# Kernel tuning notes

Hardware: AMD Instinct MI355X
Metric: run time of the kernel (lower is better)

## Reference

```python
import jax, jax.numpy as jnp
import numpy as np

D_MODEL = 1024
NUM_HEADS = 16
HEAD_DIM = D_MODEL // NUM_HEADS


def setup_inputs() -> dict:
    key = jax.random.key(0)
    ks = jax.random.split(key, 11)
    B, S, D = 2, 2048, D_MODEL
    s = 1.0 / np.sqrt(D)
    return {
        "query": jax.random.normal(ks[0], (B, S, D), jnp.float32),
        "key": jax.random.normal(ks[1], (B, S, D), jnp.float32),
        "value": jax.random.normal(ks[2], (B, S, D), jnp.float32),
        "w_q": jax.random.normal(ks[3], (D, D), jnp.float32) * s,
        "b_q": jnp.zeros((D,), jnp.float32),
        "w_k": jax.random.normal(ks[4], (D, D), jnp.float32) * s,
        "b_k": jnp.zeros((D,), jnp.float32),
        "w_v": jax.random.normal(ks[5], (D, D), jnp.float32) * s,
        "b_v": jnp.zeros((D,), jnp.float32),
        "w_o": jax.random.normal(ks[6], (D, D), jnp.float32) * s,
        "b_o": jnp.zeros((D,), jnp.float32),
    }


def reference(query, key, value, w_q, b_q, w_k, b_k, w_v, b_v, w_o, b_o):
    B, S, D = query.shape
    H, Hd = NUM_HEADS, HEAD_DIM
    # Linear layers (torch convention: x @ W.T + b)
    Q = (query @ w_q.T + b_q).reshape(B, S, H, Hd).transpose(0, 2, 1, 3)  # [B,H,S,Hd]
    K = (key @ w_k.T + b_k).reshape(B, S, H, Hd).transpose(0, 2, 1, 3)
    V = (value @ w_v.T + b_v).reshape(B, S, H, Hd).transpose(0, 2, 1, 3)
    scale = jnp.float32(np.sqrt(Hd))
    scores = jnp.einsum("bhqd,bhkd->bhqk", Q, K) / scale  # [B,H,S,S]
    attn_weights = jax.nn.softmax(scores, axis=-1)
    # dropout is identity in eval mode
    out = jnp.einsum("bhqk,bhkd->bhqd", attn_weights, V)  # [B,H,S,Hd]
    out = out.transpose(0, 2, 1, 3).reshape(B, S, D)
    out = out @ w_o.T + b_o
    return out, attn_weights
```

## Files before the change

### kernel.cpp

```cpp
#include <hip/hip_runtime.h>
#include <hip/hip_bf16.h>
#include <stdint.h>
#include <math.h>

typedef __attribute__((ext_vector_type(8))) short bf16x8;
typedef __attribute__((ext_vector_type(4))) float f32x4;
typedef __attribute__((ext_vector_type(8))) unsigned short ushort8;
typedef __attribute__((ext_vector_type(4))) unsigned short ushort4v;

#define LDS_AS(p) ((__attribute__((address_space(3))) void*)(p))
#define GLB_AS(p) ((const __attribute__((address_space(1))) void*)(p))

#define EXP2F(x) __builtin_amdgcn_exp2f(x)

__device__ __forceinline__ unsigned short f2bf(float f) {
  uint32_t u = __builtin_bit_cast(uint32_t, f);
  u += 0x7FFFu + ((u >> 16) & 1u);
  return (unsigned short)(u >> 16);
}

__global__ __launch_bounds__(256) void cvt_all_kernel(
    const float* __restrict__ q, const float* __restrict__ k, const float* __restrict__ v,
    const float* __restrict__ wq, const float* __restrict__ wk,
    const float* __restrict__ wv, const float* __restrict__ wo,
    unsigned short* __restrict__ oq, unsigned short* __restrict__ ok, unsigned short* __restrict__ ov,
    unsigned short* __restrict__ owq, unsigned short* __restrict__ owk,
    unsigned short* __restrict__ owv, unsigned short* __restrict__ owo) {
  int i = blockIdx.x * 256 + threadIdx.x;
  const float* src; unsigned short* dst; int off;
  if (i < 1572864) {
    int tsel = i / 524288; off = i - tsel * 524288;
    src = (tsel == 0) ? q : (tsel == 1) ? k : v;
    dst = (tsel == 0) ? oq : (tsel == 1) ? ok : ov;
  } else {
    int j = i - 1572864; int tsel = j >> 17; off = j & 131071;
    src = (tsel == 0) ? wq : (tsel == 1) ? wk : (tsel == 2) ? wv : wo;
    dst = (tsel == 0) ? owq : (tsel == 1) ? owk : (tsel == 2) ? owv : owo;
  }
  const f32x4* p = (const f32x4*)src + (size_t)off * 2;
  f32x4 a = p[0], b = p[1];
  ushort8 r;
  r[0] = f2bf(a[0]); r[1] = f2bf(a[1]); r[2] = f2bf(a[2]); r[3] = f2bf(a[3]);
  r[4] = f2bf(b[0]); r[5] = f2bf(b[1]); r[6] = f2bf(b[2]); r[7] = f2bf(b[3]);
  *((ushort8*)dst + off) = r;
}

template <int MODE>
__device__ __forceinline__ void gemm_bt_body(const unsigned short* __restrict__ A,
                                             const unsigned short* __restrict__ W,
                                             const float* __restrict__ bias,
                                             void* __restrict__ Cout, int N, int K) {
  __shared__ unsigned short As[128 * 64];
  __shared__ unsigned short Bs[128 * 64];
  const int t = threadIdx.x;
  const int lane = t & 63, wid = t >> 6;
  const int grp = lane >> 4, lr = lane & 15;
  const int wm = wid >> 1, wn = wid & 1;
  const int mtile = blockIdx.y * 128, ntile = blockIdx.x * 128;
  f32x4 acc[4][4] = {};
  for (int kt = 0; kt < K; kt += 64) {
    __syncthreads();
#pragma unroll
    for (int i = 0; i < 4; ++i) {
      int off = (i * 256 + t) * 16;
      int row = off >> 7, u8 = (off >> 4) & 7;
      const unsigned short* sa = A + (size_t)(mtile + row) * K + kt + u8 * 8;
      __builtin_amdgcn_global_load_lds(GLB_AS(sa), LDS_AS((char*)As + off), 16, 0, 0);
      const unsigned short* sb = W + (size_t)(ntile + row) * K + kt + u8 * 8;
      __builtin_amdgcn_global_load_lds(GLB_AS(sb), LDS_AS((char*)Bs + off), 16, 0, 0);
    }
    __syncthreads();
#pragma unroll
    for (int kc = 0; kc < 2; ++kc) {
      bf16x8 af[4], bfr[4];
#pragma unroll
      for (int mf = 0; mf < 4; ++mf) {
        int row = wm * 64 + mf * 16 + lr;
        af[mf] = *(const bf16x8*)((const char*)As + row * 128 + kc * 64 + grp * 16);
      }
#pragma unroll
      for (int nf = 0; nf < 4; ++nf) {
        int row = wn * 64 + nf * 16 + lr;
        bfr[nf] = *(const bf16x8*)((const char*)Bs + row * 128 + kc * 64 + grp * 16);
      }
#pragma unroll
      for (int mf = 0; mf < 4; ++mf)
#pragma unroll
        for (int nf = 0; nf < 4; ++nf)
          acc[mf][nf] = __builtin_amdgcn_mfma_f32_16x16x32_bf16(af[mf], bfr[nf], acc[mf][nf], 0, 0, 0);
    }
  }
#pragma unroll
  for (int nf = 0; nf < 4; ++nf) {
    int gcol = ntile + wn * 64 + nf * 16 + lr;
    float bv = bias[gcol];
#pragma unroll
    for (int mf = 0; mf < 4; ++mf) {
      int grow0 = mtile + wm * 64 + mf * 16 + grp * 4;
      if (MODE == 2) {
        ushort4v cv;
#pragma unroll
        for (int j = 0; j < 4; ++j) cv[j] = f2bf(acc[mf][nf][j] + bv);
        int bh = ((grow0 >> 11) << 4) | (gcol >> 6);
        *(ushort4v*)((unsigned short*)Cout +
                     ((size_t)(bh * 64 + (gcol & 63))) * 2048 + (grow0 & 2047)) = cv;
      } else {
#pragma unroll
        for (int j = 0; j < 4; ++j) {
          float v = acc[mf][nf][j] + bv;
          if (MODE == 1) ((unsigned short*)Cout)[(size_t)(grow0 + j) * N + gcol] = f2bf(v);
          else           ((float*)Cout)[(size_t)(grow0 + j) * N + gcol] = v;
        }
      }
    }
  }
}

__global__ __launch_bounds__(256) void gemm_qkv_kernel(
    const unsigned short* Xq, const unsigned short* Xk, const unsigned short* Xv,
    const unsigned short* Wq, const unsigned short* Wk, const unsigned short* Wv,
    const float* bq, const float* bk, const float* bv,
    unsigned short* Cq, unsigned short* Ck, unsigned short* Vt) {
  int z = blockIdx.z;
  if (z == 2)      gemm_bt_body<2>(Xv, Wv, bv, Vt, 1024, 1024);
  else if (z == 1) gemm_bt_body<1>(Xk, Wk, bk, Ck, 1024, 1024);
  else             gemm_bt_body<1>(Xq, Wq, bq, Cq, 1024, 1024);
}

__global__ __launch_bounds__(256) void gemm_out_kernel(const unsigned short* ctx,
                                                       const unsigned short* Wo,
                                                       const float* bo, float* out) {
  gemm_bt_body<0>(ctx, Wo, bo, out, 1024, 1024);
}

__global__ __launch_bounds__(256) void attn_kernel(const unsigned short* __restrict__ Qb,
                                                   const unsigned short* __restrict__ Kb,
                                                   const unsigned short* __restrict__ Vt,
                                                   float* __restrict__ attn,
                                                   unsigned short* __restrict__ ctx) {
  __shared__ unsigned short QP[4096];
  __shared__ unsigned short Ks[2][4096];
  __shared__ unsigned short Vs[2][4096];
  const int t = threadIdx.x;
  const int lane = t & 63, wid = t >> 6;
  const int grp = lane >> 4, lr = lane & 15;
  const int d0 = blockIdx.y * 32 + blockIdx.x;
  const int L = (d0 & 7) * 128 + (d0 >> 3);
  const int bh = L >> 5, qt = L & 31;
  const int b = bh >> 4, h = bh & 15;
  const int qbase = qt * 64;
  const unsigned short* Qg = Qb + ((size_t)(b * 2048 + qbase) * 1024 + h * 64);
  const unsigned short* Kg = Kb + ((size_t)(b * 2048) * 1024 + h * 64);
  const unsigned short* Vg = Vt + (size_t)bh * 64 * 2048;

  auto stageK = [&](int kt, int bs) {
#pragma unroll
    for (int i = 0; i < 2; ++i) {
      int off = (i * 256 + t) * 16;
      int row = off >> 7, u = (off >> 4) & 7, us = u ^ (row & 7);
      __builtin_amdgcn_global_load_lds(
          GLB_AS((const char*)(Kg + (size_t)kt * 64 * 1024) + row * 2048 + us * 16),
          LDS_AS((char*)Ks[bs] + off), 16, 0, 0);
    }
  };
  auto stageV = [&](int kt, int bs) {
#pragma unroll
    for (int i = 0; i < 2; ++i) {
      int off = (i * 256 + t) * 16;
      int row = off >> 7, u = (off >> 4) & 7, us = u ^ (row & 7);
      __builtin_amdgcn_global_load_lds(
          GLB_AS((const char*)(Vg + kt * 64) + row * 4096 + us * 16),
          LDS_AS((char*)Vs[bs] + off), 16, 0, 0);
    }
  };

#pragma unroll
  for (int i = 0; i < 2; ++i) {
    int off = (i * 256 + t) * 16;
    int row = off >> 7, u = (off >> 4) & 7, us = u ^ (row & 7);
    __builtin_amdgcn_global_load_lds(GLB_AS((const char*)Qg + row * 2048 + us * 16),
                                     LDS_AS((char*)QP + off), 16, 0, 0);
  }
  stageK(0, 0);
  __syncthreads();
  bf16x8 qf[2];
#pragma unroll
  for (int kc = 0; kc < 2; ++kc) {
    int row = wid * 16 + lr, c2 = kc * 64 + grp * 16;
    qf[kc] = *(const bf16x8*)((const char*)QP + (((row << 7) | c2) ^ ((row & 7) << 4)));
  }

  const float C1 = 0.18033688011112042f;
  float lsum = 0.f;
  for (int kt = 0; kt < 32; ++kt) {
    if (kt < 31) stageK(kt + 1, (kt + 1) & 1);
    const char* Kc = (const char*)Ks[kt & 1];
    f32x4 sacc[4] = {};
#pragma unroll
    for (int kc = 0; kc < 2; ++kc)
#pragma unroll
      for (int mf = 0; mf < 4; ++mf) {
        int row = mf * 16 + lr, c2 = kc * 64 + grp * 16;
        bf16x8 kf = *(const bf16x8*)(Kc + (((row << 7) | c2) ^ ((row & 7) << 4)));
        sacc[mf] = __builtin_amdgcn_mfma_f32_16x16x32_bf16(kf, qf[kc], sacc[mf], 0, 0, 0);
      }
#pragma unroll
    for (int mf = 0; mf < 4; ++mf)
#pragma unroll
      for (int j = 0; j < 4; ++j)
        lsum += EXP2F(sacc[mf][j] * C1);
    __syncthreads();
  }
  lsum += __shfl_xor(lsum, 16);
  lsum += __shfl_xor(lsum, 32);
  const float nl2l = -log2f(lsum);

  f32x4 oacc[4] = {};
  const int qg = qbase + wid * 16 + lr;
  float* arow = attn + ((size_t)bh * 2048 + qg) * 2048;
  unsigned short* Pw = &QP[wid * 1024];
  stageK(0, 0); stageV(0, 0);
  __syncthreads();
  for (int kt = 0; kt < 32; ++kt) {
    if (kt < 31) { stageK(kt + 1, (kt + 1) & 1); stageV(kt + 1, (kt + 1) & 1); }
    __builtin_amdgcn_sched_barrier(0);
    const int cur = kt & 1;
    const char* Kc = (const char*)Ks[cur];
    const char* Vc = (const char*)Vs[cur];
    f32x4 sacc[4] = {};
#pragma unroll
    for (int kc = 0; kc < 2; ++kc)
#pragma unroll
      for (int mf = 0; mf < 4; ++mf) {
        int row = mf * 16 + lr, c2 = kc * 64 + grp * 16;
        bf16x8 kf = *(const bf16x8*)(Kc + (((row << 7) | c2) ^ ((row & 7) << 4)));
        sacc[mf] = __builtin_amdgcn_mfma_f32_16x16x32_bf16(kf, qf[kc], sacc[mf], 0, 0, 0);
      }
#pragma unroll
    for (int mf = 0; mf < 4; ++mf) {
      f32x4 pv;
#pragma unroll
      for (int j = 0; j < 4; ++j) pv[j] = EXP2F(__builtin_fmaf(sacc[mf][j], C1, nl2l));
      __builtin_nontemporal_store(pv, (f32x4*)(arow + kt * 64 + mf * 16 + grp * 4));
      ushort4v pb;
#pragma unroll
      for (int j = 0; j < 4; ++j) pb[j] = f2bf(pv[j]);
      int c2 = (mf * 16 + grp * 4) * 2;
      *(ushort4v*)((char*)Pw + (((lr << 7) | c2) ^ ((lr & 7) << 4))) = pb;
    }
#pragma unroll
    for (int kc = 0; kc < 2; ++kc) {
      int c2 = kc * 64 + grp * 16;
      bf16x8 pf = *(const bf16x8*)((const char*)Pw + (((lr << 7) | c2) ^ ((lr & 7) << 4)));
#pragma unroll
      for (int df = 0; df < 4; ++df) {
        int row = df * 16 + lr;
        bf16x8 vf = *(const bf16x8*)(Vc + (((row << 7) | c2) ^ ((row & 7) << 4)));
        oacc[df] = __builtin_amdgcn_mfma_f32_16x16x32_bf16(vf, pf, oacc[df], 0, 0, 0);
      }
    }
    asm volatile("s_waitcnt vmcnt(4) lgkmcnt(0)" ::: "memory");
    __builtin_amdgcn_sched_barrier(0);
    __builtin_amdgcn_s_barrier();
  }
  unsigned short* crow = ctx + ((size_t)(b * 2048 + qg) * 1024 + h * 64);
#pragma unroll
  for (int df = 0; df < 4; ++df) {
    ushort4v cv;
#pragma unroll
    for (int j = 0; j < 4; ++j) cv[j] = f2bf(oacc[df][j]);
    *(ushort4v*)(crow + df * 16 + grp * 4) = cv;
  }
}

extern "C" void kernel_launch(void* const* d_in, const int* in_sizes, int n_in,
                              void* d_out, int out_size, void* d_ws, size_t ws_size,
                              hipStream_t stream) {
  const float* query = (const float*)d_in[0];
  const float* key   = (const float*)d_in[1];
  const float* value = (const float*)d_in[2];
  const float* w_q = (const float*)d_in[3];
  const float* b_q = (const float*)d_in[4];
  const float* w_k = (const float*)d_in[5];
  const float* b_k = (const float*)d_in[6];
  const float* w_v = (const float*)d_in[7];
  const float* b_v = (const float*)d_in[8];
  const float* w_o = (const float*)d_in[9];
  const float* b_o = (const float*)d_in[10];

  float* out  = (float*)d_out;
  float* attn = out + (size_t)2 * 2048 * 1024;

  unsigned short* ws = (unsigned short*)d_ws;
  unsigned short* Xq = ws;
  unsigned short* Xk = Xq + 4194304;
  unsigned short* Xv = Xk + 4194304;
  unsigned short* Wq = Xv + 4194304;
  unsigned short* Wk = Wq + 1048576;
  unsigned short* Wv = Wk + 1048576;
  unsigned short* Wo = Wv + 1048576;
  unsigned short* Qb = Wo + 1048576;
  unsigned short* Kb = Qb + 4194304;
  unsigned short* Vt = Kb + 4194304;
  unsigned short* ctx = Vt + 4194304;

  cvt_all_kernel<<<8192, 256, 0, stream>>>(query, key, value, w_q, w_k, w_v, w_o,
                                           Xq, Xk, Xv, Wq, Wk, Wv, Wo);
  gemm_qkv_kernel<<<dim3(8, 32, 3), 256, 0, stream>>>(Xq, Xk, Xv, Wq, Wk, Wv,
                                                      b_q, b_k, b_v, Qb, Kb, Vt);
  attn_kernel<<<dim3(32, 32), 256, 0, stream>>>(Qb, Kb, Vt, attn, ctx);
  gemm_out_kernel<<<dim3(8, 32), 256, 0, stream>>>(ctx, Wo, b_o, out);
}
```

Before: 290.2 us.

## Double attention query tile per block to reuse K/V tiles across two row groups

Each attention block now handles 128 query rows instead of 64: every wave computes two 16-row query groups, sharing each K and V fragment loaded from LDS across both. The grid is halved to 512 blocks and the P staging buffer doubles. The aim is to halve global K/V traffic and LDS fragment reads per query row. In exchange it uses more registers and LDS and launches fewer blocks, which can reduce occupancy and leave the 256 CUs less evenly loaded. The kernel is likely bound by writing the fp32 attention matrix anyway.

```diff
diff --git a/kernel.cpp b/kernel.cpp
--- a/kernel.cpp
+++ b/kernel.cpp
@@ -138,17 +138,17 @@
                                                    const unsigned short* __restrict__ Vt,
                                                    float* __restrict__ attn,
                                                    unsigned short* __restrict__ ctx) {
-  __shared__ unsigned short QP[4096];
+  __shared__ unsigned short QP[8192];
   __shared__ unsigned short Ks[2][4096];
   __shared__ unsigned short Vs[2][4096];
   const int t = threadIdx.x;
   const int lane = t & 63, wid = t >> 6;
   const int grp = lane >> 4, lr = lane & 15;
-  const int d0 = blockIdx.y * 32 + blockIdx.x;
-  const int L = (d0 & 7) * 128 + (d0 >> 3);
-  const int bh = L >> 5, qt = L & 31;
+  const int d0 = blockIdx.y * 16 + blockIdx.x;
+  const int L = (d0 & 7) * 64 + (d0 >> 3);
+  const int bh = L >> 4, qt = L & 15;
   const int b = bh >> 4, h = bh & 15;
-  const int qbase = qt * 64;
+  const int qbase = qt * 128;
   const unsigned short* Qg = Qb + ((size_t)(b * 2048 + qbase) * 1024 + h * 64);
   const unsigned short* Kg = Kb + ((size_t)(b * 2048) * 1024 + h * 64);
   const unsigned short* Vg = Vt + (size_t)bh * 64 * 2048;
@@ -175,7 +175,7 @@
   };
 
 #pragma unroll
-  for (int i = 0; i < 2; ++i) {
+  for (int i = 0; i < 4; ++i) {
     int off = (i * 256 + t) * 16;
     int row = off >> 7, u = (off >> 4) & 7, us = u ^ (row & 7);
     __builtin_amdgcn_global_load_lds(GLB_AS((const char*)Qg + row * 2048 + us * 16),
@@ -183,42 +183,57 @@
   }
   stageK(0, 0);
   __syncthreads();
-  bf16x8 qf[2];
-#pragma unroll
-  for (int kc = 0; kc < 2; ++kc) {
-    int row = wid * 16 + lr, c2 = kc * 64 + grp * 16;
-    qf[kc] = *(const bf16x8*)((const char*)QP + (((row << 7) | c2) ^ ((row & 7) << 4)));
-  }
+  bf16x8 qf[2][2];
+#pragma unroll
+  for (int qh = 0; qh < 2; ++qh)
+#pragma unroll
+    for (int kc = 0; kc < 2; ++kc) {
+      int row = wid * 32 + qh * 16 + lr, c2 = kc * 64 + grp * 16;
+      qf[qh][kc] = *(const bf16x8*)((const char*)QP + (((row << 7) | c2) ^ ((row & 7) << 4)));
+    }
 
   const float C1 = 0.18033688011112042f;
-  float lsum = 0.f;
+  float lsum[2] = {0.f, 0.f};
   for (int kt = 0; kt < 32; ++kt) {
     if (kt < 31) stageK(kt + 1, (kt + 1) & 1);
     const char* Kc = (const char*)Ks[kt & 1];
-    f32x4 sacc[4] = {};
+    bf16x8 kf[2][4];
 #pragma unroll
     for (int kc = 0; kc < 2; ++kc)
 #pragma unroll
       for (int mf = 0; mf < 4; ++mf) {
         int row = mf * 16 + lr, c2 = kc * 64 + grp * 16;
-        bf16x8 kf = *(const bf16x8*)(Kc + (((row << 7) | c2) ^ ((row & 7) << 4)));
-        sacc[mf] = __builtin_amdgcn_mfma_f32_16x16x32_bf16(kf, qf[kc], sacc[mf], 0, 0, 0);
-      }
-#pragma unroll
-    for (int mf = 0; mf < 4; ++mf)
-#pragma unroll
-      for (int j = 0; j < 4; ++j)
-        lsum += EXP2F(sacc[mf][j] * C1);
+        kf[kc][mf] = *(const bf16x8*)(Kc + (((row << 7) | c2) ^ ((row & 7) << 4)));
+      }
+#pragma unroll
+    for (int qh = 0; qh < 2; ++qh) {
+      f32x4 sacc[4] = {};
+#pragma unroll
+      for (int kc = 0; kc < 2; ++kc)
+#pragma unroll
+        for (int mf = 0; mf < 4; ++mf)
+          sacc[mf] = __builtin_amdgcn_mfma_f32_16x16x32_bf16(kf[kc][mf], qf[qh][kc], sacc[mf], 0, 0, 0);
+#pragma unroll
+      for (int mf = 0; mf < 4; ++mf)
+#pragma unroll
+        for (int j = 0; j < 4; ++j)
+          lsum[qh] += EXP2F(sacc[mf][j] * C1);
+    }
     __syncthreads();
   }
-  lsum += __shfl_xor(lsum, 16);
-  lsum += __shfl_xor(lsum, 32);
-  const float nl2l = -log2f(lsum);
-
-  f32x4 oacc[4] = {};
-  const int qg = qbase + wid * 16 + lr;
-  float* arow = attn + ((size_t)bh * 2048 + qg) * 2048;
-  unsigned short* Pw = &QP[wid * 1024];
+#pragma unroll
+  for (int qh = 0; qh < 2; ++qh) {
+    lsum[qh] += __shfl_xor(lsum[qh], 16);
+    lsum[qh] += __shfl_xor(lsum[qh], 32);
+  }
+  const float nl2l[2] = {-log2f(lsum[0]), -log2f(lsum[1])};
+
+  f32x4 oacc[2][4] = {};
+  float* arow[2];
+#pragma unroll
+  for (int qh = 0; qh < 2; ++qh)
+    arow[qh] = attn + ((size_t)bh * 2048 + qbase + wid * 32 + qh * 16 + lr) * 2048;
+  unsigned short* Pw = &QP[wid * 2048];
   stageK(0, 0); stageV(0, 0);
   __syncthreads();
   for (int kt = 0; kt < 32; ++kt) {
@@ -227,49 +242,66 @@
     const int cur = kt & 1;
     const char* Kc = (const char*)Ks[cur];
     const char* Vc = (const char*)Vs[cur];
-    f32x4 sacc[4] = {};
+    bf16x8 kf[2][4];
 #pragma unroll
     for (int kc = 0; kc < 2; ++kc)
 #pragma unroll
       for (int mf = 0; mf < 4; ++mf) {
         int row = mf * 16 + lr, c2 = kc * 64 + grp * 16;
-        bf16x8 kf = *(const bf16x8*)(Kc + (((row << 7) | c2) ^ ((row & 7) << 4)));
-        sacc[mf] = __builtin_amdgcn_mfma_f32_16x16x32_bf16(kf, qf[kc], sacc[mf], 0, 0, 0);
-      }
-#pragma unroll
-    for (int mf = 0; mf < 4; ++mf) {
-      f32x4 pv;
-#pragma unroll
-      for (int j = 0; j < 4; ++j) pv[j] = EXP2F(__builtin_fmaf(sacc[mf][j], C1, nl2l));
-      __builtin_nontemporal_store(pv, (f32x4*)(arow + kt * 64 + mf * 16 + grp * 4));
-      ushort4v pb;
-#pragma unroll
-      for (int j = 0; j < 4; ++j) pb[j] = f2bf(pv[j]);
-      int c2 = (mf * 16 + grp * 4) * 2;
-      *(ushort4v*)((char*)Pw + (((lr << 7) | c2) ^ ((lr & 7) << 4))) = pb;
+        kf[kc][mf] = *(const bf16x8*)(Kc + (((row << 7) | c2) ^ ((row & 7) << 4)));
+      }
+#pragma unroll
+    for (int qh = 0; qh < 2; ++qh) {
+      f32x4 sacc[4] = {};
+#pragma unroll
+      for (int kc = 0; kc < 2; ++kc)
+#pragma unroll
+        for (int mf = 0; mf < 4; ++mf)
+          sacc[mf] = __builtin_amdgcn_mfma_f32_16x16x32_bf16(kf[kc][mf], qf[qh][kc], sacc[mf], 0, 0, 0);
+#pragma unroll
+      for (int mf = 0; mf < 4; ++mf) {
+        f32x4 pv;
+#pragma unroll
+        for (int j = 0; j < 4; ++j) pv[j] = EXP2F(__builtin_fmaf(sacc[mf][j], C1, nl2l[qh]));
+        __builtin_nontemporal_store(pv, (f32x4*)(arow[qh] + kt * 64 + mf * 16 + grp * 4));
+        ushort4v pb;
+#pragma unroll
+        for (int j = 0; j < 4; ++j) pb[j] = f2bf(pv[j]);
+        int c2 = (mf * 16 + grp * 4) * 2;
+        *(ushort4v*)((char*)Pw + qh * 2048 + (((lr << 7) | c2) ^ ((lr & 7) << 4))) = pb;
+      }
     }
 #pragma unroll
     for (int kc = 0; kc < 2; ++kc) {
       int c2 = kc * 64 + grp * 16;
-      bf16x8 pf = *(const bf16x8*)((const char*)Pw + (((lr << 7) | c2) ^ ((lr & 7) << 4)));
+      bf16x8 vf[4];
 #pragma unroll
       for (int df = 0; df < 4; ++df) {
         int row = df * 16 + lr;
-        bf16x8 vf = *(const bf16x8*)(Vc + (((row << 7) | c2) ^ ((row & 7) << 4)));
-        oacc[df] = __builtin_amdgcn_mfma_f32_16x16x32_bf16(vf, pf, oacc[df], 0, 0, 0);
-      }
-    }
-    asm volatile("s_waitcnt vmcnt(4) lgkmcnt(0)" ::: "memory");
+        vf[df] = *(const bf16x8*)(Vc + (((row << 7) | c2) ^ ((row & 7) << 4)));
+      }
+#pragma unroll
+      for (int qh = 0; qh < 2; ++qh) {
+        bf16x8 pf = *(const bf16x8*)((const char*)Pw + qh * 2048 + (((lr << 7) | c2) ^ ((lr & 7) << 4)));
+#pragma unroll
+        for (int df = 0; df < 4; ++df)
+          oacc[qh][df] = __builtin_amdgcn_mfma_f32_16x16x32_bf16(vf[df], pf, oacc[qh][df], 0, 0, 0);
+      }
+    }
+    asm volatile("s_waitcnt vmcnt(8) lgkmcnt(0)" ::: "memory");
     __builtin_amdgcn_sched_barrier(0);
     __builtin_amdgcn_s_barrier();
   }
-  unsigned short* crow = ctx + ((size_t)(b * 2048 + qg) * 1024 + h * 64);
-#pragma unroll
-  for (int df = 0; df < 4; ++df) {
-    ushort4v cv;
-#pragma unroll
-    for (int j = 0; j < 4; ++j) cv[j] = f2bf(oacc[df][j]);
-    *(ushort4v*)(crow + df * 16 + grp * 4) = cv;
+#pragma unroll
+  for (int qh = 0; qh < 2; ++qh) {
+    unsigned short* crow = ctx + ((size_t)(b * 2048 + qbase + wid * 32 + qh * 16 + lr) * 1024 + h * 64);
+#pragma unroll
+    for (int df = 0; df < 4; ++df) {
+      ushort4v cv;
+#pragma unroll
+      for (int j = 0; j < 4; ++j) cv[j] = f2bf(oacc[qh][df][j]);
+      *(ushort4v*)(crow + df * 16 + grp * 4) = cv;
+    }
   }
 }
 
@@ -308,6 +340,6 @@
                                            Xq, Xk, Xv, Wq, Wk, Wv, Wo);
   gemm_qkv_kernel<<<dim3(8, 32, 3), 256, 0, stream>>>(Xq, Xk, Xv, Wq, Wk, Wv,
                                                       b_q, b_k, b_v, Qb, Kb, Vt);
-  attn_kernel<<<dim3(32, 32), 256, 0, stream>>>(Qb, Kb, Vt, attn, ctx);
+  attn_kernel<<<dim3(16, 32), 256, 0, stream>>>(Qb, Kb, Vt, attn, ctx);
   gemm_out_kernel<<<dim3(8, 32), 256, 0, stream>>>(ctx, Wo, b_o, out);
 }
```

After: 317.6 us (median of 2 runs). +9.4%, slower.

## Load K/V fragments directly from global into registers, dropping LDS staging

Applied to the files above, without the earlier changes.

The attention kernel no longer stages K, V and Q tiles through double-buffered shared memory with async global-to-LDS copies. Each wave now loads its MFMA operand fragments straight from global memory into registers. Only a small per-wave LDS buffer for P remains, and all block-wide barriers are removed. This cuts LDS footprint and synchronisation, but all four waves now fetch the same K/V tiles redundantly through the cache, and there is no explicit prefetch to hide load latency.

```diff
diff --git a/kernel.cpp b/kernel.cpp
--- a/kernel.cpp
+++ b/kernel.cpp
@@ -138,9 +138,7 @@
                                                    const unsigned short* __restrict__ Vt,
                                                    float* __restrict__ attn,
                                                    unsigned short* __restrict__ ctx) {
-  __shared__ unsigned short QP[4096];
-  __shared__ unsigned short Ks[2][4096];
-  __shared__ unsigned short Vs[2][4096];
+  __shared__ unsigned short Ps[4][1024];
   const int t = threadIdx.x;
   const int lane = t & 63, wid = t >> 6;
   const int grp = lane >> 4, lr = lane & 15;
@@ -148,94 +146,65 @@
   const int L = (d0 & 7) * 128 + (d0 >> 3);
   const int bh = L >> 5, qt = L & 31;
   const int b = bh >> 4, h = bh & 15;
-  const int qbase = qt * 64;
-  const unsigned short* Qg = Qb + ((size_t)(b * 2048 + qbase) * 1024 + h * 64);
-  const unsigned short* Kg = Kb + ((size_t)(b * 2048) * 1024 + h * 64);
+  const int qr = qt * 64 + wid * 16 + lr;
+  const unsigned short* Qrow = Qb + ((size_t)(b * 2048 + qr)) * 1024 + h * 64;
+  const unsigned short* Kg = Kb + (size_t)b * 2048 * 1024 + h * 64;
   const unsigned short* Vg = Vt + (size_t)bh * 64 * 2048;
 
-  auto stageK = [&](int kt, int bs) {
-#pragma unroll
-    for (int i = 0; i < 2; ++i) {
-      int off = (i * 256 + t) * 16;
-      int row = off >> 7, u = (off >> 4) & 7, us = u ^ (row & 7);
-      __builtin_amdgcn_global_load_lds(
-          GLB_AS((const char*)(Kg + (size_t)kt * 64 * 1024) + row * 2048 + us * 16),
-          LDS_AS((char*)Ks[bs] + off), 16, 0, 0);
-    }
-  };
-  auto stageV = [&](int kt, int bs) {
-#pragma unroll
-    for (int i = 0; i < 2; ++i) {
-      int off = (i * 256 + t) * 16;
-      int row = off >> 7, u = (off >> 4) & 7, us = u ^ (row & 7);
-      __builtin_amdgcn_global_load_lds(
-          GLB_AS((const char*)(Vg + kt * 64) + row * 4096 + us * 16),
-          LDS_AS((char*)Vs[bs] + off), 16, 0, 0);
-    }
-  };
-
-#pragma unroll
-  for (int i = 0; i < 2; ++i) {
-    int off = (i * 256 + t) * 16;
-    int row = off >> 7, u = (off >> 4) & 7, us = u ^ (row & 7);
-    __builtin_amdgcn_global_load_lds(GLB_AS((const char*)Qg + row * 2048 + us * 16),
-                                     LDS_AS((char*)QP + off), 16, 0, 0);
-  }
-  stageK(0, 0);
-  __syncthreads();
   bf16x8 qf[2];
 #pragma unroll
-  for (int kc = 0; kc < 2; ++kc) {
-    int row = wid * 16 + lr, c2 = kc * 64 + grp * 16;
-    qf[kc] = *(const bf16x8*)((const char*)QP + (((row << 7) | c2) ^ ((row & 7) << 4)));
-  }
+  for (int kc = 0; kc < 2; ++kc)
+    qf[kc] = *(const bf16x8*)(Qrow + kc * 32 + grp * 8);
 
   const float C1 = 0.18033688011112042f;
   float lsum = 0.f;
   for (int kt = 0; kt < 32; ++kt) {
-    if (kt < 31) stageK(kt + 1, (kt + 1) & 1);
-    const char* Kc = (const char*)Ks[kt & 1];
+    const unsigned short* Kt = Kg + (size_t)kt * 64 * 1024;
+    bf16x8 kf[2][4];
+#pragma unroll
+    for (int kc = 0; kc < 2; ++kc)
+#pragma unroll
+      for (int mf = 0; mf < 4; ++mf)
+        kf[kc][mf] = *(const bf16x8*)(Kt + (mf * 16 + lr) * 1024 + kc * 32 + grp * 8);
     f32x4 sacc[4] = {};
 #pragma unroll
     for (int kc = 0; kc < 2; ++kc)
 #pragma unroll
-      for (int mf = 0; mf < 4; ++mf) {
-        int row = mf * 16 + lr, c2 = kc * 64 + grp * 16;
-        bf16x8 kf = *(const bf16x8*)(Kc + (((row << 7) | c2) ^ ((row & 7) << 4)));
-        sacc[mf] = __builtin_amdgcn_mfma_f32_16x16x32_bf16(kf, qf[kc], sacc[mf], 0, 0, 0);
-      }
+      for (int mf = 0; mf < 4; ++mf)
+        sacc[mf] = __builtin_amdgcn_mfma_f32_16x16x32_bf16(kf[kc][mf], qf[kc], sacc[mf], 0, 0, 0);
 #pragma unroll
     for (int mf = 0; mf < 4; ++mf)
 #pragma unroll
       for (int j = 0; j < 4; ++j)
         lsum += EXP2F(sacc[mf][j] * C1);
-    __syncthreads();
   }
   lsum += __shfl_xor(lsum, 16);
   lsum += __shfl_xor(lsum, 32);
   const float nl2l = -log2f(lsum);
 
   f32x4 oacc[4] = {};
-  const int qg = qbase + wid * 16 + lr;
-  float* arow = attn + ((size_t)bh * 2048 + qg) * 2048;
-  unsigned short* Pw = &QP[wid * 1024];
-  stageK(0, 0); stageV(0, 0);
-  __syncthreads();
+  float* arow = attn + ((size_t)bh * 2048 + qr) * 2048;
+  unsigned short* Pw = &Ps[wid][0];
   for (int kt = 0; kt < 32; ++kt) {
-    if (kt < 31) { stageK(kt + 1, (kt + 1) & 1); stageV(kt + 1, (kt + 1) & 1); }
-    __builtin_amdgcn_sched_barrier(0);
-    const int cur = kt & 1;
-    const char* Kc = (const char*)Ks[cur];
-    const char* Vc = (const char*)Vs[cur];
+    const unsigned short* Kt = Kg + (size_t)kt * 64 * 1024;
+    bf16x8 kf[2][4];
+#pragma unroll
+    for (int kc = 0; kc < 2; ++kc)
+#pragma unroll
+      for (int mf = 0; mf < 4; ++mf)
+        kf[kc][mf] = *(const bf16x8*)(Kt + (mf * 16 + lr) * 1024 + kc * 32 + grp * 8);
+    bf16x8 vf[2][4];
+#pragma unroll
+    for (int kc = 0; kc < 2; ++kc)
+#pragma unroll
+      for (int df = 0; df < 4; ++df)
+        vf[kc][df] = *(const bf16x8*)(Vg + (df * 16 + lr) * 2048 + kt * 64 + kc * 32 + grp * 8);
     f32x4 sacc[4] = {};
 #pragma unroll
     for (int kc = 0; kc < 2; ++kc)
 #pragma unroll
-      for (int mf = 0; mf < 4; ++mf) {
-        int row = mf * 16 + lr, c2 = kc * 64 + grp * 16;
-        bf16x8 kf = *(const bf16x8*)(Kc + (((row << 7) | c2) ^ ((row & 7) << 4)));
-        sacc[mf] = __builtin_amdgcn_mfma_f32_16x16x32_bf16(kf, qf[kc], sacc[mf], 0, 0, 0);
-      }
+      for (int mf = 0; mf < 4; ++mf)
+        sacc[mf] = __builtin_amdgcn_mfma_f32_16x16x32_bf16(kf[kc][mf], qf[kc], sacc[mf], 0, 0, 0);
 #pragma unroll
     for (int mf = 0; mf < 4; ++mf) {
       f32x4 pv;
@@ -253,17 +222,11 @@
       int c2 = kc * 64 + grp * 16;
       bf16x8 pf = *(const bf16x8*)((const char*)Pw + (((lr << 7) | c2) ^ ((lr & 7) << 4)));
 #pragma unroll
-      for (int df = 0; df < 4; ++df) {
-        int row = df * 16 + lr;
-        bf16x8 vf = *(const bf16x8*)(Vc + (((row << 7) | c2) ^ ((row & 7) << 4)));
-        oacc[df] = __builtin_amdgcn_mfma_f32_16x16x32_bf16(vf, pf, oacc[df], 0, 0, 0);
-      }
-    }
-    asm volatile("s_waitcnt vmcnt(4) lgkmcnt(0)" ::: "memory");
-    __builtin_amdgcn_sched_barrier(0);
-    __builtin_amdgcn_s_barrier();
-  }
-  unsigned short* crow = ctx + ((size_t)(b * 2048 + qg) * 1024 + h * 64);
+      for (int df = 0; df < 4; ++df)
+        oacc[df] = __builtin_amdgcn_mfma_f32_16x16x32_bf16(vf[kc][df], pf, oacc[df], 0, 0, 0);
+    }
+  }
+  unsigned short* crow = ctx + ((size_t)(b * 2048 + qr) * 1024 + h * 64);
 #pragma unroll
   for (int df = 0; df < 4; ++df) {
     ushort4v cv;
```

Result: slower. 451.0 us (+55.4%).
